# Performance work log

Measured on AMD Instinct MI355X. Metric: run time of the kernel, lower is better.

Reference implementation:

```python
import jax, jax.numpy as jnp
import numpy as np

SIZE = (4096, 4096)   # self.size
SIGMA = 1.0           # blur_sigma
NOISE_STD = 0.01      # noise_std


def _gauss_kernel(sigma):
    # scipy.ndimage.gaussian_filter: radius = int(truncate*sigma + 0.5), truncate=4.0
    r = int(4.0 * sigma + 0.5)
    x = np.arange(-r, r + 1, dtype=np.float32)
    k = np.exp(-0.5 * (x / sigma) ** 2)
    k = k / k.sum()
    return jnp.asarray(k), r


def _blur(img, sigma):
    # img: [C, H, W]; separable Gaussian, scipy mode='reflect' == jnp symmetric pad
    k, r = _gauss_kernel(sigma)
    x = jnp.pad(img, ((0, 0), (r, r), (r, r)), mode='symmetric')
    x = x[:, None]  # [C, 1, H+2r, W+2r] (NCHW)
    kh = k.reshape(1, 1, -1, 1)
    kw = k.reshape(1, 1, 1, -1)
    x = jax.lax.conv_general_dilated(x, kh, (1, 1), 'VALID')
    x = jax.lax.conv_general_dilated(x, kw, (1, 1), 'VALID')
    return x[:, 0]  # [C, H, W]


def setup_inputs() -> dict:
    key = jax.random.key(0)
    k1, k2 = jax.random.split(key)
    img = jax.random.normal(k1, (1, 2048, 2048), dtype=jnp.float32)
    noise = jax.random.normal(k2, (1,) + SIZE, dtype=jnp.float32)
    return {"img": img, "noise": noise}


def reference(img, noise):
    # bilinear resize, align_corners=False == jax half-pixel linear resize
    img = jax.image.resize(img, (img.shape[0],) + SIZE, method='linear')
    img = jnp.flip(img, axis=2)   # horizontal flip
    img = jnp.flip(img, axis=1)   # vertical flip
    img = jnp.rot90(img, k=1, axes=(1, 2))  # rot90, k fixed to 1
    img = img + noise * NOISE_STD
    img = _blur(img, SIGMA)
    img = jnp.log1p(jnp.clip(img, 0.0))  # clamp(min=0) then log1p
    return img
```

## Files before the change

kernel.cpp:

```cpp
#include <hip/hip_runtime.h>
#include <math.h>

#define N     4096
#define NIMG  2048
#define TX    56
#define TY    32
#define DW    64
#define DH    40
#define IPR   36
#define IPP   25
#define STP   41
#define VP    65
#define S2P   57

#define KW0 0.00013383063f
#define KW1 0.00443186160f
#define KW2 0.05399112800f
#define KW3 0.24197144000f
#define KW4 0.39894346870f

__device__ __forceinline__ int symi(int g) {
    g = (g < 0) ? (-1 - g) : g;
    g = (g >= N) ? (2 * N - 1 - g) : g;
    return g;
}

__global__ __launch_bounds__(256, 8)
void TensorAugment_79216376807666_kernel(const float* __restrict__ img,
                                         const float* __restrict__ noise,
                                         float* __restrict__ out) {
    __shared__ float ST[DW * STP];
    __shared__ float UN[TY * VP];
    float* const IP = UN;
    float* const V  = UN;

    const int tid  = threadIdx.x;
    const int lane = tid & 63;
    const int wave = tid >> 6;
    const int bx = blockIdx.x, by = blockIdx.y;
    const int x0 = bx * TX;
    const int y0 = by * TY;
    const bool interior = (bx >= 1) && (bx <= 72) && (by >= 1) && (by <= 126);

    const float kk[9] = {KW0, KW1, KW2, KW3, KW4, KW3, KW2, KW1, KW0};

    int gxa = x0 - 4, gxb = x0 + DW - 5;
    int mxa = symi(gxa), mxb = symi(gxb);
    int gxmin = min(mxa, mxb), gxmax = max(mxa, mxb);
    if (gxa <= 0) gxmin = 0;
    if (gxb >= N - 1) gxmax = N - 1;
    int umin = (N - 1) - gxmax, umax = (N - 1) - gxmin;
    int r0min = (umin - 1) >> 1;
    int r0max = (umax - 1) >> 1;
    int nrows = r0max - r0min + 2;

    int gya = y0 - 4, gyb = y0 + DH - 5;
    int mya = symi(gya), myb = symi(gyb);
    int gymin = min(mya, myb), gymax = max(mya, myb);
    if (gya <= 0) gymin = 0;
    if (gyb >= N - 1) gymax = N - 1;
    int c0min = (gymin - 1) >> 1;
    int c0max = (gymax - 1) >> 1;
    int ncols = c0max - c0min + 2;

    {
        int c = tid & 31;
        for (int r = tid >> 5; r < nrows; r += 8) {
            if (c < ncols) {
                int ir = min(max(r0min + r, 0), NIMG - 1);
                int ic = min(max(c0min + c, 0), NIMG - 1);
                IP[r * IPP + c] = img[ir * NIMG + ic];
            }
        }
    }
    __syncthreads();

    if (interior) {
        int g  = lane & 15;
        int rr = lane >> 4;
        int sbase = (30 - 2 * g) * IPP;
        const float* npz = noise + (size_t)(y0 - 4) * N + (x0 - 4) + 4 * g;
#pragma unroll
        for (int it = 0; it < 3; ++it) {
            int row = it * 16 + wave * 4 + rr;
            if (row < DH) {
                int jc  = (row + 1) >> 1;
                float wc1 = (row & 1) ? 0.25f : 0.75f;
                float wc0 = 1.0f - wc1;
                float4 nv = *reinterpret_cast<const float4*>(npz + (size_t)row * N);
                int b = sbase + jc;
                float t0 = fmaf(wc0, IP[b],           wc1 * IP[b + 1]);
                float t1 = fmaf(wc0, IP[b + IPP],     wc1 * IP[b + IPP + 1]);
                float t2 = fmaf(wc0, IP[b + 2 * IPP], wc1 * IP[b + 2 * IPP + 1]);
                float t3 = fmaf(wc0, IP[b + 3 * IPP], wc1 * IP[b + 3 * IPP + 1]);
                float D0 = fmaf(0.75f, t2, 0.25f * t3);
                float D1 = fmaf(0.25f, t1, 0.75f * t2);
                float D2 = fmaf(0.75f, t1, 0.25f * t2);
                float D3 = fmaf(0.25f, t0, 0.75f * t1);
                int sb = (4 * g) * STP + row;
                ST[sb]           = fmaf(0.01f, nv.x, D0);
                ST[sb + STP]     = fmaf(0.01f, nv.y, D1);
                ST[sb + 2 * STP] = fmaf(0.01f, nv.z, D2);
                ST[sb + 3 * STP] = fmaf(0.01f, nv.w, D3);
            }
        }
    } else {
        int c   = lane;
        int gxm = symi(x0 - 4 + c);
        int u   = (N - 1) - gxm;
        int r0  = (u - 1) >> 1;
        float wr1 = (u & 1) ? 0.25f : 0.75f;
        float wr0 = 1.0f - wr1;
        int a0 = (r0 - r0min) * IPP;
#pragma unroll
        for (int k = 0; k < 10; ++k) {
            int row = wave + 4 * k;
            int gym = symi(y0 - 4 + row);
            int c0  = (gym - 1) >> 1;
            float wc1 = (gym & 1) ? 0.25f : 0.75f;
            float wc0 = 1.0f - wc1;
            int jc = c0 - c0min;
            float nv = noise[gym * N + gxm];
            float f0 = IP[a0 + jc],       f1 = IP[a0 + jc + 1];
            float f2 = IP[a0 + IPP + jc], f3 = IP[a0 + IPP + jc + 1];
            float top = fmaf(wc0, f0, wc1 * f1);
            float bot = fmaf(wc0, f2, wc1 * f3);
            ST[c * STP + row] = fmaf(wr0, top, wr1 * bot) + 0.01f * nv;
        }
    }
    __syncthreads();

    {
        int c  = lane;
        int rb = wave * 8;
        float win[16];
        int ab = c * STP + rb;
#pragma unroll
        for (int k = 0; k < 16; ++k) win[k] = ST[ab + k];
#pragma unroll
        for (int j = 0; j < 8; ++j) {
            float acc = 0.0f;
#pragma unroll
            for (int i = 0; i < 9; ++i) acc = fmaf(kk[i], win[j + i], acc);
            V[(rb + j) * VP + c] = acc;
        }
    }
    __syncthreads();

    {
        int r = tid >> 3;
        int s = tid & 7;
        float w2[15];
        int vb = r * VP + s * 7;
#pragma unroll
        for (int k = 0; k < 15; ++k) w2[k] = V[vb + k];
#pragma unroll
        for (int j = 0; j < 7; ++j) {
            float acc = 0.0f;
#pragma unroll
            for (int i = 0; i < 9; ++i) acc = fmaf(kk[i], w2[j + i], acc);
            acc = fmaxf(acc, 0.0f);
            ST[r * S2P + s * 7 + j] = __logf(1.0f + acc);
        }
    }
    __syncthreads();

    for (int r = wave; r < TY; r += 4) {
        int gx = x0 + lane;
        if (lane < TX && gx < N)
            out[(size_t)(y0 + r) * N + gx] = ST[r * S2P + lane];
    }
}

extern "C" void kernel_launch(void* const* d_in, const int* in_sizes, int n_in,
                              void* d_out, int out_size, void* d_ws, size_t ws_size,
                              hipStream_t stream) {
    const float* img   = (const float*)d_in[0];
    const float* noise = (const float*)d_in[1];
    float* out = (float*)d_out;

    dim3 grid((N + TX - 1) / TX, N / TY);
    TensorAugment_79216376807666_kernel<<<grid, 256, 0, stream>>>(img, noise, out);
}
```

Measured before the change: 144.5 us.

## Prefetch noise before image staging and remap blocks across XCDs

The interior path's noise float4 loads are issued at kernel start, before the image patch is staged into shared memory, so their latency overlaps the staging load and barrier. Block indices are remapped so that each of the 8 XCDs gets a contiguous band of 16 tile rows, which is meant to improve L2 locality of the halo rows. Launch bounds drop from 8 to 4 blocks per SM to leave room for the extra live registers, and the S2P shared-memory padding changes from 57 to 59. Risks are lower occupancy and more register pressure.

Measured after the change: 144.0 us. Within noise of the previous version (-0.3%).

```diff
diff --git a/kernel.cpp b/kernel.cpp
--- a/kernel.cpp
+++ b/kernel.cpp
@@ -7,11 +7,12 @@
 #define TY    32
 #define DW    64
 #define DH    40
-#define IPR   36
 #define IPP   25
 #define STP   41
 #define VP    65
-#define S2P   57
+#define S2P   59
+#define GBX   74
+#define GBY   128
 
 #define KW0 0.00013383063f
 #define KW1 0.00443186160f
@@ -25,7 +26,7 @@
     return g;
 }
 
-__global__ __launch_bounds__(256, 8)
+__global__ __launch_bounds__(256, 4)
 void TensorAugment_79216376807666_kernel(const float* __restrict__ img,
                                          const float* __restrict__ noise,
                                          float* __restrict__ out) {
@@ -37,12 +38,30 @@
     const int tid  = threadIdx.x;
     const int lane = tid & 63;
     const int wave = tid >> 6;
-    const int bx = blockIdx.x, by = blockIdx.y;
+
+    int b   = blockIdx.y * GBX + blockIdx.x;
+    int xcd = b & 7;
+    int i   = b >> 3;
+    int bx  = i % GBX;
+    int by  = xcd * 16 + i / GBX;
+
     const int x0 = bx * TX;
     const int y0 = by * TY;
     const bool interior = (bx >= 1) && (bx <= 72) && (by >= 1) && (by <= 126);
 
     const float kk[9] = {KW0, KW1, KW2, KW3, KW4, KW3, KW2, KW1, KW0};
+
+    const int g  = lane & 15;
+    const int rr = lane >> 4;
+    const int rowbase = wave * 4 + rr;
+    float4 nv0, nv1, nv2;
+    if (interior) {
+        const float* npz = noise + (size_t)(y0 - 4) * N + (x0 - 4) + 4 * g;
+        nv0 = *reinterpret_cast<const float4*>(npz + (size_t)rowbase * N);
+        nv1 = *reinterpret_cast<const float4*>(npz + (size_t)(rowbase + 16) * N);
+        if (rowbase + 32 < DH)
+            nv2 = *reinterpret_cast<const float4*>(npz + (size_t)(rowbase + 32) * N);
+    }
 
     int gxa = x0 - 4, gxb = x0 + DW - 5;
     int mxa = symi(gxa), mxb = symi(gxb);
@@ -76,23 +95,21 @@
     __syncthreads();
 
     if (interior) {
-        int g  = lane & 15;
-        int rr = lane >> 4;
         int sbase = (30 - 2 * g) * IPP;
-        const float* npz = noise + (size_t)(y0 - 4) * N + (x0 - 4) + 4 * g;
+        float4 nvv[3] = {nv0, nv1, nv2};
 #pragma unroll
         for (int it = 0; it < 3; ++it) {
-            int row = it * 16 + wave * 4 + rr;
+            int row = it * 16 + rowbase;
             if (row < DH) {
                 int jc  = (row + 1) >> 1;
                 float wc1 = (row & 1) ? 0.25f : 0.75f;
                 float wc0 = 1.0f - wc1;
-                float4 nv = *reinterpret_cast<const float4*>(npz + (size_t)row * N);
-                int b = sbase + jc;
-                float t0 = fmaf(wc0, IP[b],           wc1 * IP[b + 1]);
-                float t1 = fmaf(wc0, IP[b + IPP],     wc1 * IP[b + IPP + 1]);
-                float t2 = fmaf(wc0, IP[b + 2 * IPP], wc1 * IP[b + 2 * IPP + 1]);
-                float t3 = fmaf(wc0, IP[b + 3 * IPP], wc1 * IP[b + 3 * IPP + 1]);
+                float4 nv = nvv[it];
+                int bofs = sbase + jc;
+                float t0 = fmaf(wc0, IP[bofs],           wc1 * IP[bofs + 1]);
+                float t1 = fmaf(wc0, IP[bofs + IPP],     wc1 * IP[bofs + IPP + 1]);
+                float t2 = fmaf(wc0, IP[bofs + 2 * IPP], wc1 * IP[bofs + 2 * IPP + 1]);
+                float t3 = fmaf(wc0, IP[bofs + 3 * IPP], wc1 * IP[bofs + 3 * IPP + 1]);
                 float D0 = fmaf(0.75f, t2, 0.25f * t3);
                 float D1 = fmaf(0.25f, t1, 0.75f * t2);
                 float D2 = fmaf(0.75f, t1, 0.25f * t2);
@@ -120,12 +137,12 @@
             float wc1 = (gym & 1) ? 0.25f : 0.75f;
             float wc0 = 1.0f - wc1;
             int jc = c0 - c0min;
-            float nv = noise[gym * N + gxm];
+            float nvs = noise[(size_t)gym * N + gxm];
             float f0 = IP[a0 + jc],       f1 = IP[a0 + jc + 1];
             float f2 = IP[a0 + IPP + jc], f3 = IP[a0 + IPP + jc + 1];
             float top = fmaf(wc0, f0, wc1 * f1);
             float bot = fmaf(wc0, f2, wc1 * f3);
-            ST[c * STP + row] = fmaf(wr0, top, wr1 * bot) + 0.01f * nv;
+            ST[c * STP + row] = fmaf(wr0, top, wr1 * bot) + 0.01f * nvs;
         }
     }
     __syncthreads();
@@ -141,7 +158,7 @@
         for (int j = 0; j < 8; ++j) {
             float acc = 0.0f;
 #pragma unroll
-            for (int i = 0; i < 9; ++i) acc = fmaf(kk[i], win[j + i], acc);
+            for (int i2 = 0; i2 < 9; ++i2) acc = fmaf(kk[i2], win[j + i2], acc);
             V[(rb + j) * VP + c] = acc;
         }
     }
@@ -158,7 +175,7 @@
         for (int j = 0; j < 7; ++j) {
             float acc = 0.0f;
 #pragma unroll
-            for (int i = 0; i < 9; ++i) acc = fmaf(kk[i], w2[j + i], acc);
+            for (int i2 = 0; i2 < 9; ++i2) acc = fmaf(kk[i2], w2[j + i2], acc);
             acc = fmaxf(acc, 0.0f);
             ST[r * S2P + s * 7 + j] = __logf(1.0f + acc);
         }
@@ -179,6 +196,6 @@
     const float* noise = (const float*)d_in[1];
     float* out = (float*)d_out;
 
-    dim3 grid((N + TX - 1) / TX, N / TY);
+    dim3 grid(GBX, GBY);
     TensorAugment_79216376807666_kernel<<<grid, 256, 0, stream>>>(img, noise, out);
 }
```
